# Kernel optimization log

Measured on AMD Instinct MI355X. Metric: run time of the kernel, lower is better.

Reference implementation:

```python
import jax, jax.numpy as jnp
import numpy as np

NFEATS = 768; NHIDS = 768; H = 8; HD = NHIDS // H
NT = 32768; NC = 32768; NS = 32768; DEG = 8; E = NT * DEG
ALPHA = 0.2  # LeakyReLU negative slope


def setup_inputs() -> dict:
    key = jax.random.key(0)
    ks = jax.random.split(key, 16)
    f32 = jnp.float32
    dst = jnp.repeat(jnp.arange(NT, dtype=jnp.int32), DEG)  # uniform in-degree mailbox
    return {
        'h': jax.random.normal(ks[0], (NT, NFEATS), f32),
        'hb_c_src': jax.random.normal(ks[1], (NC, NHIDS), f32),
        'hb_s_src': jax.random.normal(ks[2], (NS, NHIDS), f32),
        'Wg': jax.random.normal(ks[3], (H, NFEATS, HD), f32) * 0.05,
        'bg': jnp.zeros((H, HD), f32),
        'ag': jax.random.normal(ks[4], (H, 2 * HD), f32) * 0.1,
        'agb': jnp.zeros((H,), f32),
        'Wx': jax.random.normal(ks[5], (H, NHIDS, HD), f32) * 0.05,
        'bx': jnp.zeros((H, HD), f32),
        'ax': jax.random.normal(ks[6], (H, 2 * HD), f32) * 0.1,
        'axb': jnp.zeros((H,), f32),
        'Wih': jax.random.normal(ks[7], (3 * NHIDS, NHIDS), f32) * 0.02,
        'Whh': jax.random.normal(ks[8], (3 * NHIDS, NHIDS), f32) * 0.02,
        'bih': jnp.zeros((3 * NHIDS,), f32),
        'bhh': jnp.zeros((3 * NHIDS,), f32),
        'intra_src': jax.random.randint(ks[9], (E,), 0, NT, jnp.int32),
        'intra_dst': dst,
        'c_src': jax.random.randint(ks[10], (E,), 0, NC, jnp.int32),
        'c_dst': dst,
        's_src': jax.random.randint(ks[11], (E,), 0, NS, jnp.int32),
        's_dst': dst,
    }


def _attend(Wh_s, Wh_d, src, dst, a, ab, n_dst):
    """Multi-head GAT edge attention + segment softmax + weighted aggregation.
    Wh_s: [Ns,H,D] src projections, Wh_d: [Nd,H,D] dst projections.
    a([Wh_src||Wh_dst]) decomposed as a_src.Wh_src + a_dst.Wh_dst + bias."""
    D = Wh_s.shape[-1]
    e = (jnp.einsum('nhd,hd->nh', Wh_s, a[:, :D])[src]
         + jnp.einsum('nhd,hd->nh', Wh_d, a[:, D:])[dst] + ab)  # [E,H]
    e = jax.nn.leaky_relu(e, ALPHA)
    m = jax.ops.segment_max(e, dst, num_segments=n_dst)
    ex = jnp.exp(e - m[dst])
    den = jax.ops.segment_sum(ex, dst, num_segments=n_dst)
    att = ex / den[dst]  # per-dst softmax over incoming edges (DGL mailbox softmax)
    out = jax.ops.segment_sum(Wh_s[src] * att[..., None], dst, num_segments=n_dst)
    return out.reshape(n_dst, H * D)  # concat heads


def _forward(h, hb_c_src, hb_s_src, Wg, bg, ag, agb, Wx, bx, ax, axb,
             Wih, Whh, bih, bhh, intra_src, intra_dst, c_src, c_dst, s_src, s_dst):
    n = h.shape[0]
    # intra-turn GAT (x = self.gat(g, t)); dropout is identity in eval mode
    Wh = jnp.einsum('nf,hfd->nhd', h, Wg) + bg
    x = _attend(Wh, Wh, intra_src, intra_dst, ag, agb, n)
    # cross-turn inversed GAT; dst nodes' 'hb' feature is the fresh gat output x;
    # counter_bw and support_bw share the same xgat weights.
    Wx_d = jnp.einsum('nf,hfd->nhd', x, Wx) + bx
    Wc_s = jnp.einsum('nf,hfd->nhd', hb_c_src, Wx) + bx
    h_c = _attend(Wc_s, Wx_d, c_src, c_dst, ax, axb, n)
    Ws_s = jnp.einsum('nf,hfd->nhd', hb_s_src, Wx) + bx
    h_s = _attend(Ws_s, Wx_d, s_src, s_dst, ax, axb, n)
    hid = 0.5 * h_c + 0.5 * h_s
    # GRUCell(x, hid)
    gi = x @ Wih.T + bih
    gh = hid @ Whh.T + bhh
    ir, iz, inn = jnp.split(gi, 3, axis=1)
    hr, hz, hn = jnp.split(gh, 3, axis=1)
    r = jax.nn.sigmoid(ir + hr)
    z = jax.nn.sigmoid(iz + hz)
    cand = jnp.tanh(inn + r * hn)
    return (1.0 - z) * cand + z * hid


def reference(h, hb_c_src, hb_s_src, Wg, bg, ag, agb, Wx, bx, ax, axb,
              Wih, Whh, bih, bhh, intra_src, intra_dst, c_src, c_dst, s_src, s_dst):
    return _forward(h, hb_c_src, hb_s_src, Wg, bg, ag, agb, Wx, bx, ax, axb,
                    Wih, Whh, bih, bhh, intra_src, intra_dst, c_src, c_dst, s_src, s_dst)
```

## Files before the change

### kernel.cpp

```cpp
#include <hip/hip_runtime.h>
#include <hip/hip_bf16.h>
#include <math.h>

#define NT 32768
#define HD 96
#define DEG 8
#define NE (NT * DEG)
#define LRELU_ALPHA 0.2f
#define CH 8192

typedef __attribute__((ext_vector_type(8))) short bf16x8;
typedef __attribute__((ext_vector_type(8))) unsigned short u16x8;
typedef __attribute__((ext_vector_type(4))) unsigned short u16x4;
typedef __attribute__((ext_vector_type(4))) float f32x4;

__device__ __forceinline__ unsigned short f2bf(float x) {
    union { float f; unsigned u; } v; v.f = x;
    unsigned r = v.u + 0x7FFFu + ((v.u >> 16) & 1u);
    return (unsigned short)(r >> 16);
}
__device__ __forceinline__ float bf2f(unsigned short u) {
    union { unsigned u; float f; } v; v.u = ((unsigned)u) << 16; return v.f;
}

__device__ __forceinline__ void gload_lds16(const void* g, void* l) {
    __builtin_amdgcn_global_load_lds(
        (const __attribute__((address_space(1))) void*)g,
        (__attribute__((address_space(3))) void*)l, 16, 0, 0);
}


__global__ void packWT(const float* __restrict__ W, unsigned short* __restrict__ T) {
    int idx = blockIdx.x * 256 + threadIdx.x;
    if (idx >= 768 * 768) return;
    int c = idx / 768, f = idx % 768;
    T[idx] = f2bf(W[(size_t)(c / HD) * 768 * HD + (size_t)f * HD + (c % HD)]);
}

__global__ void cvt_bf8(const float* __restrict__ X, unsigned short* __restrict__ Y, int n8) {
    int i = blockIdx.x * 256 + threadIdx.x;
    if (i >= n8) return;
    float4 a = ((const float4*)X)[2 * i];
    float4 b = ((const float4*)X)[2 * i + 1];
    u16x8 p;
    p[0] = f2bf(a.x); p[1] = f2bf(a.y); p[2] = f2bf(a.z); p[3] = f2bf(a.w);
    p[4] = f2bf(b.x); p[5] = f2bf(b.y); p[6] = f2bf(b.z); p[7] = f2bf(b.w);
    ((u16x8*)Y)[i] = p;
}

__global__ __launch_bounds__(256, 2) void mgemm_bb(
    const unsigned short* __restrict__ A, const unsigned short* __restrict__ BT,
    const float* __restrict__ bias, unsigned short* __restrict__ C,
    int M, int N, int K) {
    __shared__ unsigned short Alds[128 * 32];
    __shared__ unsigned short Blds[128 * 32];
    const int tid = threadIdx.x;
    const int w = tid >> 6, l = tid & 63;
    const int wr = w >> 1, wc = w & 1;
    const int lrow = l & 15, lk = l >> 4;

    const int nx = gridDim.x;
    const int nwg = nx * gridDim.y;
    int lin = blockIdx.y * nx + blockIdx.x;
    if ((nwg & 7) == 0) lin = (lin & 7) * (nwg >> 3) + (lin >> 3);
    const int bm = lin / nx, bn = lin % nx;

    const unsigned short* asrc[2];
    const unsigned short* bsrc[2];
    #pragma unroll
    for (int q = 0; q < 2; q++) {
        int idx = q * 256 + tid;
        int r = idx >> 2, s = idx & 3;
        int kw = s ^ ((r >> 1) & 3);
        asrc[q] = A  + (size_t)(bm * 128 + r) * K + kw * 8;
        bsrc[q] = BT + (size_t)(bn * 128 + r) * K + kw * 8;
    }

    f32x4 acc[4][4] = {};

    for (int k0 = 0; k0 < K; k0 += 32) {
        __syncthreads();
        gload_lds16(asrc[0] + k0, &Alds[(0 * 256 + w * 64) * 8]);
        gload_lds16(asrc[1] + k0, &Alds[(1 * 256 + w * 64) * 8]);
        gload_lds16(bsrc[0] + k0, &Blds[(0 * 256 + w * 64) * 8]);
        gload_lds16(bsrc[1] + k0, &Blds[(1 * 256 + w * 64) * 8]);
        __syncthreads();
        bf16x8 af[4], bfv[4];
        #pragma unroll
        for (int i = 0; i < 4; i++) {
            int r = wr * 64 + i * 16 + lrow;
            int s = lk ^ ((r >> 1) & 3);
            af[i] = *(const bf16x8*)(&Alds[r * 32 + s * 8]);
        }
        #pragma unroll
        for (int j = 0; j < 4; j++) {
            int r = wc * 64 + j * 16 + lrow;
            int s = lk ^ ((r >> 1) & 3);
            bfv[j] = *(const bf16x8*)(&Blds[r * 32 + s * 8]);
        }
        #pragma unroll
        for (int i = 0; i < 4; i++)
            #pragma unroll
            for (int j = 0; j < 4; j++)
                acc[i][j] = __builtin_amdgcn_mfma_f32_16x16x32_bf16(af[i], bfv[j], acc[i][j], 0, 0, 0);
    }

    const size_t crow0 = (size_t)bm * 128 + wr * 64;
    const int ccol0 = bn * 128 + wc * 64;
    #pragma unroll
    for (int j = 0; j < 4; j++) {
        int col = ccol0 + j * 16 + lrow;
        float bv = bias[col];
        #pragma unroll
        for (int i = 0; i < 4; i++) {
            size_t row = crow0 + i * 16 + lk * 4;
            #pragma unroll
            for (int e = 0; e < 4; e++)
                C[(row + e) * N + col] = f2bf(acc[i][j][e] + bv);
        }
    }
}

__global__ __launch_bounds__(256) void escore(
    const unsigned short* __restrict__ X, const float* __restrict__ a,
    int half, float* __restrict__ sc) {
    __shared__ float av[768];
    for (int t = threadIdx.x; t < 768; t += 256) {
        int hh = t / HD, d = t % HD;
        av[t] = a[hh * 2 * HD + half * HD + d];
    }
    __syncthreads();
    int idx = blockIdx.x * 256 + threadIdx.x;
    int row = idx >> 3, hh = idx & 7;
    const unsigned short* xp = X + (size_t)row * 768 + hh * HD;
    const float* ap = av + hh * HD;
    float s = 0.f;
    #pragma unroll
    for (int q = 0; q < 12; q++) {
        u16x8 v = *(const u16x8*)(xp + q * 8);
        #pragma unroll
        for (int e = 0; e < 8; e++) s += bf2f(v[e]) * ap[q * 8 + e];
    }
    sc[idx] = s;
}

__global__ __launch_bounds__(256) void attend_agg(
    const unsigned short* __restrict__ Whs, const float* __restrict__ es,
    const float* __restrict__ ed, const float* __restrict__ ab,
    const int* __restrict__ src, const int* __restrict__ dst,
    unsigned short* __restrict__ out, float alpha, float beta) {
    const int wv = threadIdx.x >> 6, l = threadIdx.x & 63;
    const int seg = blockIdx.x * 4 + wv;
    const int hh = l >> 3, j = l & 7;
    int sj = src[seg * 8 + j];
    int dnode = dst[seg * 8];
    float e = es[(size_t)sj * 8 + hh] + ed[(size_t)dnode * 8 + hh] + ab[hh];
    e = e > 0.f ? e : LRELU_ALPHA * e;
    float m = e;
    #pragma unroll
    for (int o = 1; o < 8; o <<= 1) m = fmaxf(m, __shfl_xor(m, o, 64));
    float ex = expf(e - m);
    float s = ex;
    #pragma unroll
    for (int o = 1; o < 8; o <<= 1) s += __shfl_xor(s, o, 64);
    float att = ex / s;

    #pragma unroll
    for (int u = 0; u < 3; u++) {
        int c = 4 * l + 256 * u;
        int h = c / HD;
        float acc0 = 0.f, acc1 = 0.f, acc2 = 0.f, acc3 = 0.f;
        #pragma unroll
        for (int j2 = 0; j2 < 8; j2++) {
            float a = __shfl(att, h * 8 + j2, 64);
            int sid = __shfl(sj, j2, 64);
            u16x4 v = *(const u16x4*)(Whs + (size_t)sid * 768 + c);
            acc0 += a * bf2f(v[0]); acc1 += a * bf2f(v[1]);
            acc2 += a * bf2f(v[2]); acc3 += a * bf2f(v[3]);
        }
        u16x4 r;
        unsigned short* op = out + (size_t)dnode * 768 + c;
        if (beta != 0.f) {
            u16x4 pv = *(const u16x4*)op;
            r[0] = f2bf(alpha * acc0 + beta * bf2f(pv[0]));
            r[1] = f2bf(alpha * acc1 + beta * bf2f(pv[1]));
            r[2] = f2bf(alpha * acc2 + beta * bf2f(pv[2]));
            r[3] = f2bf(alpha * acc3 + beta * bf2f(pv[3]));
        } else {
            r[0] = f2bf(alpha * acc0); r[1] = f2bf(alpha * acc1);
            r[2] = f2bf(alpha * acc2); r[3] = f2bf(alpha * acc3);
        }
        *(u16x4*)op = r;
    }
}

__global__ __launch_bounds__(256) void gru_elem(
    const unsigned short* __restrict__ gi, const unsigned short* __restrict__ gh,
    const unsigned short* __restrict__ hid, float* __restrict__ out) {
    int idx = blockIdx.x * 256 + threadIdx.x;
    int nrow = idx / 96, c8 = (idx % 96) * 8;
    const unsigned short* gip = gi + (size_t)nrow * 2304 + c8;
    const unsigned short* ghp = gh + (size_t)nrow * 2304 + c8;
    u16x8 vir = *(const u16x8*)(gip);
    u16x8 viz = *(const u16x8*)(gip + 768);
    u16x8 vin = *(const u16x8*)(gip + 1536);
    u16x8 vhr = *(const u16x8*)(ghp);
    u16x8 vhz = *(const u16x8*)(ghp + 768);
    u16x8 vhn = *(const u16x8*)(ghp + 1536);
    u16x8 vh  = *(const u16x8*)(hid + (size_t)nrow * 768 + c8);
    float res[8];
    #pragma unroll
    for (int e = 0; e < 8; e++) {
        float r = 1.f / (1.f + expf(-(bf2f(vir[e]) + bf2f(vhr[e]))));
        float z = 1.f / (1.f + expf(-(bf2f(viz[e]) + bf2f(vhz[e]))));
        float cand = tanhf(bf2f(vin[e]) + r * bf2f(vhn[e]));
        res[e] = (1.f - z) * cand + z * bf2f(vh[e]);
    }
    float* op = out + (size_t)nrow * 768 + c8;
    *(float4*)(op)     = make_float4(res[0], res[1], res[2], res[3]);
    *(float4*)(op + 4) = make_float4(res[4], res[5], res[6], res[7]);
}

extern "C" void kernel_launch(void* const* d_in, const int* in_sizes, int n_in,
                              void* d_out, int out_size, void* d_ws, size_t ws_size,
                              hipStream_t stream) {
    const float* h    = (const float*)d_in[0];
    const float* hbc  = (const float*)d_in[1];
    const float* hbs  = (const float*)d_in[2];
    const float* Wg   = (const float*)d_in[3];
    const float* bg   = (const float*)d_in[4];
    const float* ag   = (const float*)d_in[5];
    const float* agb  = (const float*)d_in[6];
    const float* Wx   = (const float*)d_in[7];
    const float* bx   = (const float*)d_in[8];
    const float* ax   = (const float*)d_in[9];
    const float* axb  = (const float*)d_in[10];
    const float* Wih  = (const float*)d_in[11];
    const float* Whh  = (const float*)d_in[12];
    const float* bih  = (const float*)d_in[13];
    const float* bhh  = (const float*)d_in[14];
    const int* i_src  = (const int*)d_in[15];
    const int* i_dst  = (const int*)d_in[16];
    const int* c_src  = (const int*)d_in[17];
    const int* c_dst  = (const int*)d_in[18];
    const int* s_src  = (const int*)d_in[19];
    const int* s_dst  = (const int*)d_in[20];
    float* out = (float*)d_out;

    const size_t SZ = (size_t)NT * 768;
    unsigned short* Xb  = (unsigned short*)d_ws;
    unsigned short* Hdb = Xb + SZ;
    unsigned short* GIb = Hdb + SZ;
    unsigned short* GHb = GIb + (size_t)CH * 2304;
    unsigned short* AB  = GIb;
    unsigned short* W2gT = GHb + (size_t)CH * 2304;
    unsigned short* W2xT = W2gT + 768 * 768;
    unsigned short* WihB = W2xT + 768 * 768;
    unsigned short* WhhB = WihB + 2304 * 768;
    float* ES  = (float*)(WhhB + 2304 * 768);
    float* ED  = ES + NE;
    float* ESI = ED + NE;
    float* EDI = ESI + NE;
    unsigned short* Pb = (unsigned short*)d_out;

    dim3 blk(256);
    packWT<<<(768 * 768 + 255) / 256, blk, 0, stream>>>(Wg, W2gT);
    packWT<<<(768 * 768 + 255) / 256, blk, 0, stream>>>(Wx, W2xT);
    cvt_bf8<<<(2304 * 768 / 8 + 255) / 256, blk, 0, stream>>>(Wih, WihB, 2304 * 768 / 8);
    cvt_bf8<<<(2304 * 768 / 8 + 255) / 256, blk, 0, stream>>>(Whh, WhhB, 2304 * 768 / 8);

    dim3 g768(6, NT / 128);
    const int n8 = (int)(SZ / 8);
    const int cvtg = (n8 + 255) / 256;

    cvt_bf8<<<cvtg, blk, 0, stream>>>(h, AB, n8);
    mgemm_bb<<<g768, blk, 0, stream>>>(AB, W2gT, bg, Pb, NT, 768, 768);
    escore<<<NE / 256, blk, 0, stream>>>(Pb, ag, 0, ESI);
    escore<<<NE / 256, blk, 0, stream>>>(Pb, ag, 1, EDI);
    attend_agg<<<NT / 4, blk, 0, stream>>>(Pb, ESI, EDI, agb, i_src, i_dst, Xb, 1.f, 0.f);
    mgemm_bb<<<g768, blk, 0, stream>>>(Xb, W2xT, bx, Pb, NT, 768, 768);
    escore<<<NE / 256, blk, 0, stream>>>(Pb, ax, 1, ED);
    cvt_bf8<<<cvtg, blk, 0, stream>>>(hbc, AB, n8);
    mgemm_bb<<<g768, blk, 0, stream>>>(AB, W2xT, bx, Pb, NT, 768, 768);
    escore<<<NE / 256, blk, 0, stream>>>(Pb, ax, 0, ES);
    attend_agg<<<NT / 4, blk, 0, stream>>>(Pb, ES, ED, axb, c_src, c_dst, Hdb, 0.5f, 0.f);
    cvt_bf8<<<cvtg, blk, 0, stream>>>(hbs, AB, n8);
    mgemm_bb<<<g768, blk, 0, stream>>>(AB, W2xT, bx, Pb, NT, 768, 768);
    escore<<<NE / 256, blk, 0, stream>>>(Pb, ax, 0, ES);
    attend_agg<<<NT / 4, blk, 0, stream>>>(Pb, ES, ED, axb, s_src, s_dst, Hdb, 0.5f, 1.f);

    dim3 gch(2304 / 128, CH / 128);
    for (int c0 = 0; c0 < NT; c0 += CH) {
        mgemm_bb<<<gch, blk, 0, stream>>>(Xb  + (size_t)c0 * 768, WihB, bih, GIb, CH, 2304, 768);
        mgemm_bb<<<gch, blk, 0, stream>>>(Hdb + (size_t)c0 * 768, WhhB, bhh, GHb, CH, 2304, 768);
        gru_elem<<<(CH * 96) / 256, blk, 0, stream>>>(GIb, GHb, Hdb + (size_t)c0 * 768, out + (size_t)c0 * 768);
    }
}
```

Before: 1.031 ms.

## Double-buffer GEMM LDS, fuse score kernels and counter/support attention

The GEMM now double-buffers its LDS tiles, issuing the next K-tile's global-to-LDS load before computing the current one, and asks for higher occupancy through its launch bounds. The two intra-GAT score passes become one kernel that reads each projection row once. The counter and support attentions are merged into one kernel that aggregates both and writes the averaged result, dropping a read-modify-write of Hdb and one launch. This needs an extra workspace buffer for the second projection, and the doubled LDS plus higher occupancy target may limit registers.

Result: faster. 1.010 ms (-2.0%).

```diff
diff --git a/kernel.cpp b/kernel.cpp
--- a/kernel.cpp
+++ b/kernel.cpp
@@ -48,12 +48,12 @@
     ((u16x8*)Y)[i] = p;
 }
 
-__global__ __launch_bounds__(256, 2) void mgemm_bb(
+__global__ __launch_bounds__(256, 4) void mgemm_bb(
     const unsigned short* __restrict__ A, const unsigned short* __restrict__ BT,
     const float* __restrict__ bias, unsigned short* __restrict__ C,
     int M, int N, int K) {
-    __shared__ unsigned short Alds[128 * 32];
-    __shared__ unsigned short Blds[128 * 32];
+    __shared__ unsigned short Alds[2][128 * 32];
+    __shared__ unsigned short Blds[2][128 * 32];
     const int tid = threadIdx.x;
     const int w = tid >> 6, l = tid & 63;
     const int wr = w >> 1, wc = w & 1;
@@ -75,28 +75,38 @@
         asrc[q] = A  + (size_t)(bm * 128 + r) * K + kw * 8;
         bsrc[q] = BT + (size_t)(bn * 128 + r) * K + kw * 8;
     }
+    const int ldst = (w * 64) * 8;
+
+    gload_lds16(asrc[0], &Alds[0][ldst]);
+    gload_lds16(asrc[1], &Alds[0][2048 + ldst]);
+    gload_lds16(bsrc[0], &Blds[0][ldst]);
+    gload_lds16(bsrc[1], &Blds[0][2048 + ldst]);
 
     f32x4 acc[4][4] = {};
-
-    for (int k0 = 0; k0 < K; k0 += 32) {
+    const int nt = K >> 5;
+
+    for (int t = 0; t < nt; ++t) {
+        const int cur = t & 1;
         __syncthreads();
-        gload_lds16(asrc[0] + k0, &Alds[(0 * 256 + w * 64) * 8]);
-        gload_lds16(asrc[1] + k0, &Alds[(1 * 256 + w * 64) * 8]);
-        gload_lds16(bsrc[0] + k0, &Blds[(0 * 256 + w * 64) * 8]);
-        gload_lds16(bsrc[1] + k0, &Blds[(1 * 256 + w * 64) * 8]);
-        __syncthreads();
+        if (t + 1 < nt) {
+            const int k1 = (t + 1) << 5;
+            gload_lds16(asrc[0] + k1, &Alds[cur ^ 1][ldst]);
+            gload_lds16(asrc[1] + k1, &Alds[cur ^ 1][2048 + ldst]);
+            gload_lds16(bsrc[0] + k1, &Blds[cur ^ 1][ldst]);
+            gload_lds16(bsrc[1] + k1, &Blds[cur ^ 1][2048 + ldst]);
+        }
         bf16x8 af[4], bfv[4];
         #pragma unroll
         for (int i = 0; i < 4; i++) {
             int r = wr * 64 + i * 16 + lrow;
             int s = lk ^ ((r >> 1) & 3);
-            af[i] = *(const bf16x8*)(&Alds[r * 32 + s * 8]);
+            af[i] = *(const bf16x8*)(&Alds[cur][r * 32 + s * 8]);
         }
         #pragma unroll
         for (int j = 0; j < 4; j++) {
             int r = wc * 64 + j * 16 + lrow;
             int s = lk ^ ((r >> 1) & 3);
-            bfv[j] = *(const bf16x8*)(&Blds[r * 32 + s * 8]);
+            bfv[j] = *(const bf16x8*)(&Blds[cur][r * 32 + s * 8]);
         }
         #pragma unroll
         for (int i = 0; i < 4; i++)
@@ -119,6 +129,36 @@
                 C[(row + e) * N + col] = f2bf(acc[i][j][e] + bv);
         }
     }
+}
+
+__global__ __launch_bounds__(256) void escore2(
+    const unsigned short* __restrict__ X, const float* __restrict__ a,
+    float* __restrict__ s0out, float* __restrict__ s1out) {
+    __shared__ float av0[768], av1[768];
+    for (int t = threadIdx.x; t < 768; t += 256) {
+        int hh = t / HD, d = t % HD;
+        av0[t] = a[hh * 2 * HD + d];
+        av1[t] = a[hh * 2 * HD + HD + d];
+    }
+    __syncthreads();
+    int idx = blockIdx.x * 256 + threadIdx.x;
+    int row = idx >> 3, hh = idx & 7;
+    const unsigned short* xp = X + (size_t)row * 768 + hh * HD;
+    const float* a0 = av0 + hh * HD;
+    const float* a1 = av1 + hh * HD;
+    float s0 = 0.f, s1 = 0.f;
+    #pragma unroll
+    for (int q = 0; q < 12; q++) {
+        u16x8 v = *(const u16x8*)(xp + q * 8);
+        #pragma unroll
+        for (int e = 0; e < 8; e++) {
+            float x = bf2f(v[e]);
+            s0 += x * a0[q * 8 + e];
+            s1 += x * a1[q * 8 + e];
+        }
+    }
+    s0out[idx] = s0;
+    s1out[idx] = s1;
 }
 
 __global__ __launch_bounds__(256) void escore(
@@ -148,7 +188,7 @@
     const unsigned short* __restrict__ Whs, const float* __restrict__ es,
     const float* __restrict__ ed, const float* __restrict__ ab,
     const int* __restrict__ src, const int* __restrict__ dst,
-    unsigned short* __restrict__ out, float alpha, float beta) {
+    unsigned short* __restrict__ out) {
     const int wv = threadIdx.x >> 6, l = threadIdx.x & 63;
     const int seg = blockIdx.x * 4 + wv;
     const int hh = l >> 3, j = l & 7;
@@ -179,18 +219,72 @@
             acc2 += a * bf2f(v[2]); acc3 += a * bf2f(v[3]);
         }
         u16x4 r;
-        unsigned short* op = out + (size_t)dnode * 768 + c;
-        if (beta != 0.f) {
-            u16x4 pv = *(const u16x4*)op;
-            r[0] = f2bf(alpha * acc0 + beta * bf2f(pv[0]));
-            r[1] = f2bf(alpha * acc1 + beta * bf2f(pv[1]));
-            r[2] = f2bf(alpha * acc2 + beta * bf2f(pv[2]));
-            r[3] = f2bf(alpha * acc3 + beta * bf2f(pv[3]));
-        } else {
-            r[0] = f2bf(alpha * acc0); r[1] = f2bf(alpha * acc1);
-            r[2] = f2bf(alpha * acc2); r[3] = f2bf(alpha * acc3);
-        }
-        *(u16x4*)op = r;
+        r[0] = f2bf(acc0); r[1] = f2bf(acc1); r[2] = f2bf(acc2); r[3] = f2bf(acc3);
+        *(u16x4*)(out + (size_t)dnode * 768 + c) = r;
+    }
+}
+
+__global__ __launch_bounds__(256) void attend2(
+    const unsigned short* __restrict__ Wc, const unsigned short* __restrict__ Ws,
+    const float* __restrict__ esC, const float* __restrict__ esS,
+    const float* __restrict__ ed, const float* __restrict__ ab,
+    const int* __restrict__ csrc, const int* __restrict__ ssrc,
+    const int* __restrict__ dst, unsigned short* __restrict__ outH) {
+    const int wv = threadIdx.x >> 6, l = threadIdx.x & 63;
+    const int seg = blockIdx.x * 4 + wv;
+    const int hh = l >> 3, j = l & 7;
+    int cj = csrc[seg * 8 + j];
+    int sj = ssrc[seg * 8 + j];
+    int dnode = dst[seg * 8];
+    float edv = ed[(size_t)dnode * 8 + hh] + ab[hh];
+
+    float eC = esC[(size_t)cj * 8 + hh] + edv;
+    eC = eC > 0.f ? eC : LRELU_ALPHA * eC;
+    float mC = eC;
+    #pragma unroll
+    for (int o = 1; o < 8; o <<= 1) mC = fmaxf(mC, __shfl_xor(mC, o, 64));
+    float exC = expf(eC - mC);
+    float sC = exC;
+    #pragma unroll
+    for (int o = 1; o < 8; o <<= 1) sC += __shfl_xor(sC, o, 64);
+    float attC = exC / sC;
+
+    float eS = esS[(size_t)sj * 8 + hh] + edv;
+    eS = eS > 0.f ? eS : LRELU_ALPHA * eS;
+    float mS = eS;
+    #pragma unroll
+    for (int o = 1; o < 8; o <<= 1) mS = fmaxf(mS, __shfl_xor(mS, o, 64));
+    float exS = expf(eS - mS);
+    float sS = exS;
+    #pragma unroll
+    for (int o = 1; o < 8; o <<= 1) sS += __shfl_xor(sS, o, 64);
+    float attS = exS / sS;
+
+    #pragma unroll
+    for (int u = 0; u < 3; u++) {
+        int c = 4 * l + 256 * u;
+        int h = c / HD;
+        float acc0 = 0.f, acc1 = 0.f, acc2 = 0.f, acc3 = 0.f;
+        #pragma unroll
+        for (int j2 = 0; j2 < 8; j2++) {
+            float a = __shfl(attC, h * 8 + j2, 64);
+            int sid = __shfl(cj, j2, 64);
+            u16x4 v = *(const u16x4*)(Wc + (size_t)sid * 768 + c);
+            acc0 += a * bf2f(v[0]); acc1 += a * bf2f(v[1]);
+            acc2 += a * bf2f(v[2]); acc3 += a * bf2f(v[3]);
+        }
+        #pragma unroll
+        for (int j2 = 0; j2 < 8; j2++) {
+            float a = __shfl(attS, h * 8 + j2, 64);
+            int sid = __shfl(sj, j2, 64);
+            u16x4 v = *(const u16x4*)(Ws + (size_t)sid * 768 + c);
+            acc0 += a * bf2f(v[0]); acc1 += a * bf2f(v[1]);
+            acc2 += a * bf2f(v[2]); acc3 += a * bf2f(v[3]);
+        }
+        u16x4 r;
+        r[0] = f2bf(0.5f * acc0); r[1] = f2bf(0.5f * acc1);
+        r[2] = f2bf(0.5f * acc2); r[3] = f2bf(0.5f * acc3);
+        *(u16x4*)(outH + (size_t)dnode * 768 + c) = r;
     }
 }
 
@@ -261,6 +355,7 @@
     float* ED  = ES + NE;
     float* ESI = ED + NE;
     float* EDI = ESI + NE;
+    unsigned short* P2b = (unsigned short*)(EDI + NE);
     unsigned short* Pb = (unsigned short*)d_out;
 
     dim3 blk(256);
@@ -275,19 +370,17 @@
 
     cvt_bf8<<<cvtg, blk, 0, stream>>>(h, AB, n8);
     mgemm_bb<<<g768, blk, 0, stream>>>(AB, W2gT, bg, Pb, NT, 768, 768);
-    escore<<<NE / 256, blk, 0, stream>>>(Pb, ag, 0, ESI);
-    escore<<<NE / 256, blk, 0, stream>>>(Pb, ag, 1, EDI);
-    attend_agg<<<NT / 4, blk, 0, stream>>>(Pb, ESI, EDI, agb, i_src, i_dst, Xb, 1.f, 0.f);
+    escore2<<<NE / 256, blk, 0, stream>>>(Pb, ag, ESI, EDI);
+    attend_agg<<<NT / 4, blk, 0, stream>>>(Pb, ESI, EDI, agb, i_src, i_dst, Xb);
     mgemm_bb<<<g768, blk, 0, stream>>>(Xb, W2xT, bx, Pb, NT, 768, 768);
     escore<<<NE / 256, blk, 0, stream>>>(Pb, ax, 1, ED);
     cvt_bf8<<<cvtg, blk, 0, stream>>>(hbc, AB, n8);
     mgemm_bb<<<g768, blk, 0, stream>>>(AB, W2xT, bx, Pb, NT, 768, 768);
     escore<<<NE / 256, blk, 0, stream>>>(Pb, ax, 0, ES);
-    attend_agg<<<NT / 4, blk, 0, stream>>>(Pb, ES, ED, axb, c_src, c_dst, Hdb, 0.5f, 0.f);
     cvt_bf8<<<cvtg, blk, 0, stream>>>(hbs, AB, n8);
-    mgemm_bb<<<g768, blk, 0, stream>>>(AB, W2xT, bx, Pb, NT, 768, 768);
-    escore<<<NE / 256, blk, 0, stream>>>(Pb, ax, 0, ES);
-    attend_agg<<<NT / 4, blk, 0, stream>>>(Pb, ES, ED, axb, s_src, s_dst, Hdb, 0.5f, 1.f);
+    mgemm_bb<<<g768, blk, 0, stream>>>(AB, W2xT, bx, P2b, NT, 768, 768);
+    escore<<<NE / 256, blk, 0, stream>>>(P2b, ax, 0, ESI);
+    attend2<<<NT / 4, blk, 0, stream>>>(Pb, P2b, ES, ESI, ED, axb, c_src, s_src, c_dst, Hdb);
 
     dim3 gch(2304 / 128, CH / 128);
     for (int c0 = 0; c0 < NT; c0 += CH) {
```
